# Optimization experiments

Hardware: AMD Instinct MI355X
Metric: run time of the kernel (lower is better)

## Reference

```python
import jax, jax.numpy as jnp
import numpy as np

N_SRC = 100_000
N_NODES = 1_000_000
N_NEIGH = 20
RAW_DIM = 256
NEIGH_DIM = 128
MSG_DIM = 128


def setup_inputs() -> dict:
    key = jax.random.key(0)
    ks = jax.random.split(key, 8)
    s = 0.05
    return {
        "raw_messages": jax.random.normal(ks[0], (N_SRC, RAW_DIM), dtype=jnp.float32),
        "neighbors": jax.random.randint(ks[1], (N_SRC, N_NEIGH), 0, N_NODES, dtype=jnp.int64),
        "memory": jax.random.normal(ks[2], (N_NODES, NEIGH_DIM), dtype=jnp.float32),
        "W1": jax.random.normal(ks[3], (RAW_DIM, RAW_DIM // 2), dtype=jnp.float32) * s,
        "b1": jnp.zeros((RAW_DIM // 2,), dtype=jnp.float32),
        "W2": jax.random.normal(ks[4], (RAW_DIM // 2, MSG_DIM), dtype=jnp.float32) * s,
        "b2": jnp.zeros((MSG_DIM,), dtype=jnp.float32),
        "Wn": jax.random.normal(ks[5], (NEIGH_DIM, MSG_DIM), dtype=jnp.float32) * s,
        "bn": jnp.zeros((MSG_DIM,), dtype=jnp.float32),
    }


def reference(raw_messages, neighbors, memory, W1, b1, W2, b2, Wn, bn):
    # Gather neighbor memories: [N, K, D_neigh]
    neighbor_memories = memory[neighbors]
    # Mean-pool over the K sampled neighbors: [N, D_neigh]
    neighbor_agg = neighbor_memories.mean(axis=1)
    # message_sum MLP: Linear -> ReLU -> Linear -> ReLU
    h = jax.nn.relu(raw_messages @ W1 + b1)
    a = jax.nn.relu(h @ W2 + b2)
    # neighbor_sum MLP: Linear -> ReLU
    b = jax.nn.relu(neighbor_agg @ Wn + bn)
    return a + b
```

## Files before the change

### kernel.cpp

```cpp
#include <hip/hip_runtime.h>

#define N_SRC   100000
#define N_NEIGH 20
#define DRAW    256
#define DH      128
#define DMSG    128
#define DNEI    128
#define LDS_PAD 8

typedef __bf16 bf16x8 __attribute__((ext_vector_type(8)));
typedef float  floatx4 __attribute__((ext_vector_type(4)));

__global__ void convert_weights(const float* __restrict__ W1,
                                const float* __restrict__ W2,
                                const float* __restrict__ Wn,
                                __bf16* __restrict__ W1t,
                                __bf16* __restrict__ W2t,
                                __bf16* __restrict__ Wnt) {
    int i = blockIdx.x * 256 + threadIdx.x;
    if (i < 32768) {
        int n = i >> 8, k = i & 255;
        W1t[i] = (__bf16)W1[k * 128 + n];
    } else if (i < 49152) {
        int j = i - 32768;
        int n = j >> 7, k = j & 127;
        W2t[j] = (__bf16)W2[k * 128 + n];
    } else {
        int j = i - 49152;
        int n = j >> 7, k = j & 127;
        Wnt[j] = (__bf16)Wn[k * 128 + n];
    }
}

__global__ __launch_bounds__(256)
void fused_kernel(const float* __restrict__ raw,
                  const int*   __restrict__ neigh,
                  const float* __restrict__ memv,
                  const float* __restrict__ b1,
                  const float* __restrict__ b2,
                  const float* __restrict__ bn,
                  const __bf16* __restrict__ W1t,
                  const __bf16* __restrict__ W2t,
                  const __bf16* __restrict__ Wnt,
                  float* __restrict__ out) {
    __shared__ __bf16 agg [64][DNEI + LDS_PAD];
    __shared__ __bf16 hbuf[64][DH   + LDS_PAD];

    const int tid = threadIdx.x;
    const int s0  = blockIdx.x * 64;

    {
        const int grp = tid >> 5;
        const int l32 = tid & 31;
        for (int sl = grp; sl < 64; sl += 8) {
            const int s = s0 + sl;
            float4 acc = make_float4(0.f, 0.f, 0.f, 0.f);
            if (s < N_SRC) {
                int myidx = 0;
                if (l32 < N_NEIGH) myidx = neigh[s * N_NEIGH + l32];
                #pragma unroll
                for (int n = 0; n < N_NEIGH; ++n) {
                    int idx = __shfl(myidx, n, 32);
                    const float4* row =
                        reinterpret_cast<const float4*>(memv + (size_t)idx * DNEI);
                    float4 v = row[l32];
                    acc.x += v.x; acc.y += v.y; acc.z += v.z; acc.w += v.w;
                }
                const float inv = 1.0f / N_NEIGH;
                acc.x *= inv; acc.y *= inv; acc.z *= inv; acc.w *= inv;
            }
            __bf16* dst = &agg[sl][l32 * 4];
            dst[0] = (__bf16)acc.x; dst[1] = (__bf16)acc.y;
            dst[2] = (__bf16)acc.z; dst[3] = (__bf16)acc.w;
        }
    }

    const int lane = tid & 63;
    const int wave = tid >> 6;
    const int mr   = lane & 15;
    const int quad = lane >> 4;

    {
        int rowg = s0 + wave * 16 + mr;
        int rowc = rowg < N_SRC ? rowg : N_SRC - 1;
        const float* ar = raw + (size_t)rowc * DRAW;

        floatx4 acc[8];
        #pragma unroll
        for (int nt = 0; nt < 8; ++nt) { floatx4 z = {0.f,0.f,0.f,0.f}; acc[nt] = z; }

        #pragma unroll
        for (int kk = 0; kk < DRAW; kk += 32) {
            const int kb = kk + quad * 8;
            float4 a0 = *reinterpret_cast<const float4*>(ar + kb);
            float4 a1 = *reinterpret_cast<const float4*>(ar + kb + 4);
            bf16x8 af;
            af[0]=(__bf16)a0.x; af[1]=(__bf16)a0.y; af[2]=(__bf16)a0.z; af[3]=(__bf16)a0.w;
            af[4]=(__bf16)a1.x; af[5]=(__bf16)a1.y; af[6]=(__bf16)a1.z; af[7]=(__bf16)a1.w;
            #pragma unroll
            for (int nt = 0; nt < 8; ++nt) {
                bf16x8 bf = *reinterpret_cast<const bf16x8*>(
                    W1t + (nt * 16 + mr) * DRAW + kb);
                acc[nt] = __builtin_amdgcn_mfma_f32_16x16x32_bf16(af, bf, acc[nt], 0, 0, 0);
            }
        }
        #pragma unroll
        for (int nt = 0; nt < 8; ++nt) {
            const int col  = nt * 16 + mr;
            const float bias = b1[col];
            #pragma unroll
            for (int r = 0; r < 4; ++r) {
                int mrow = wave * 16 + quad * 4 + r;
                float v = acc[nt][r] + bias;
                hbuf[mrow][col] = (__bf16)(v > 0.f ? v : 0.f);
            }
        }
    }

    __syncthreads();

    {
        floatx4 acc2[8], acc3[8];
        #pragma unroll
        for (int nt = 0; nt < 8; ++nt) {
            floatx4 z = {0.f,0.f,0.f,0.f}; acc2[nt] = z; acc3[nt] = z;
        }

        #pragma unroll
        for (int kk = 0; kk < DH; kk += 32) {
            const int kb = kk + quad * 8;
            bf16x8 af2 = *reinterpret_cast<const bf16x8*>(&hbuf[wave * 16 + mr][kb]);
            bf16x8 af3 = *reinterpret_cast<const bf16x8*>(&agg [wave * 16 + mr][kb]);
            #pragma unroll
            for (int nt = 0; nt < 8; ++nt) {
                bf16x8 bw2 = *reinterpret_cast<const bf16x8*>(
                    W2t + (nt * 16 + mr) * DH + kb);
                acc2[nt] = __builtin_amdgcn_mfma_f32_16x16x32_bf16(af2, bw2, acc2[nt], 0, 0, 0);
                bf16x8 bw3 = *reinterpret_cast<const bf16x8*>(
                    Wnt + (nt * 16 + mr) * DNEI + kb);
                acc3[nt] = __builtin_amdgcn_mfma_f32_16x16x32_bf16(af3, bw3, acc3[nt], 0, 0, 0);
            }
        }

        #pragma unroll
        for (int nt = 0; nt < 8; ++nt) {
            const int col = nt * 16 + mr;
            const float bb2 = b2[col];
            const float bbn = bn[col];
            #pragma unroll
            for (int r = 0; r < 4; ++r) {
                int rowl = wave * 16 + quad * 4 + r;
                int rowg = s0 + rowl;
                if (rowg < N_SRC) {
                    float va = acc2[nt][r] + bb2; va = va > 0.f ? va : 0.f;
                    float vb = acc3[nt][r] + bbn; vb = vb > 0.f ? vb : 0.f;
                    out[(size_t)rowg * DMSG + col] = va + vb;
                }
            }
        }
    }
}

extern "C" void kernel_launch(void* const* d_in, const int* in_sizes, int n_in,
                              void* d_out, int out_size, void* d_ws, size_t ws_size,
                              hipStream_t stream) {
    const float* raw   = (const float*)d_in[0];
    const int*   neigh = (const int*)  d_in[1];
    const float* memv  = (const float*)d_in[2];
    const float* W1    = (const float*)d_in[3];
    const float* b1    = (const float*)d_in[4];
    const float* W2    = (const float*)d_in[5];
    const float* b2    = (const float*)d_in[6];
    const float* Wn    = (const float*)d_in[7];
    const float* bn    = (const float*)d_in[8];
    float* out = (float*)d_out;

    __bf16* W1t = (__bf16*)d_ws;
    __bf16* W2t = W1t + 32768;
    __bf16* Wnt = W2t + 16384;

    convert_weights<<<dim3(256), dim3(256), 0, stream>>>(W1, W2, Wn, W1t, W2t, Wnt);

    const int nblocks = (N_SRC + 63) / 64;
    fused_kernel<<<dim3(nblocks), dim3(256), 0, stream>>>(
        raw, neigh, memv, b1, b2, bn, W1t, W2t, Wnt, out);
}
```

Measured before the change: 888.7 us.

## Split neighbor gather into separate kernel with batched loads, stage aggregate in workspace

Moves the neighbor gather and mean into a standalone kernel that issues ten independent row loads at a time per 32-lane group, then writes a bf16 aggregate buffer to the workspace. A second kernel runs the MLPs and reads that aggregate into shared memory. The goal is more memory-level parallelism on the random gather, which dominates the traffic, and decoupling it from the MFMA work. In exchange it adds an extra launch plus a write and read of a 25 MB bf16 intermediate, and it falls back to the fused kernel when the workspace is too small.

```diff
diff --git a/kernel.cpp b/kernel.cpp
--- a/kernel.cpp
+++ b/kernel.cpp
@@ -9,6 +9,7 @@
 #define LDS_PAD 8
 
 typedef __bf16 bf16x8 __attribute__((ext_vector_type(8)));
+typedef __bf16 bf16x4 __attribute__((ext_vector_type(4)));
 typedef float  floatx4 __attribute__((ext_vector_type(4)));
 
 __global__ void convert_weights(const float* __restrict__ W1,
@@ -33,6 +34,151 @@
 }
 
 __global__ __launch_bounds__(256)
+void gather_kernel(const int* __restrict__ neigh,
+                   const float* __restrict__ memv,
+                   __bf16* __restrict__ agg) {
+    const int gid = (blockIdx.x * 256 + threadIdx.x) >> 5;
+    const int l32 = threadIdx.x & 31;
+    if (gid >= N_SRC) return;
+
+    int myidx = 0;
+    if (l32 < N_NEIGH) myidx = neigh[gid * N_NEIGH + l32];
+
+    float4 acc = make_float4(0.f, 0.f, 0.f, 0.f);
+    float4 v[10];
+    #pragma unroll
+    for (int b = 0; b < 2; ++b) {
+        #pragma unroll
+        for (int j = 0; j < 10; ++j) {
+            int idx = __shfl(myidx, b * 10 + j, 32);
+            v[j] = reinterpret_cast<const float4*>(memv + (size_t)idx * DNEI)[l32];
+        }
+        #pragma unroll
+        for (int j = 0; j < 10; ++j) {
+            acc.x += v[j].x; acc.y += v[j].y; acc.z += v[j].z; acc.w += v[j].w;
+        }
+    }
+    const float inv = 1.0f / N_NEIGH;
+    bf16x4 o;
+    o[0] = (__bf16)(acc.x * inv); o[1] = (__bf16)(acc.y * inv);
+    o[2] = (__bf16)(acc.z * inv); o[3] = (__bf16)(acc.w * inv);
+    *reinterpret_cast<bf16x4*>(agg + (size_t)gid * DNEI + l32 * 4) = o;
+}
+
+__global__ __launch_bounds__(256)
+void mlp_kernel(const float* __restrict__ raw,
+                const __bf16* __restrict__ aggG,
+                const float* __restrict__ b1,
+                const float* __restrict__ b2,
+                const float* __restrict__ bn,
+                const __bf16* __restrict__ W1t,
+                const __bf16* __restrict__ W2t,
+                const __bf16* __restrict__ Wnt,
+                float* __restrict__ out) {
+    __shared__ __bf16 agg [64][DNEI + LDS_PAD];
+    __shared__ __bf16 hbuf[64][DH   + LDS_PAD];
+
+    const int tid = threadIdx.x;
+    const int s0  = blockIdx.x * 64;
+
+    {
+        #pragma unroll
+        for (int c = tid; c < 64 * 16; c += 256) {
+            int r = c >> 4, off = (c & 15) * 8;
+            if (s0 + r < N_SRC) {
+                *reinterpret_cast<bf16x8*>(&agg[r][off]) =
+                    *reinterpret_cast<const bf16x8*>(aggG + (size_t)(s0 + r) * DNEI + off);
+            }
+        }
+    }
+
+    const int lane = tid & 63;
+    const int wave = tid >> 6;
+    const int mr   = lane & 15;
+    const int quad = lane >> 4;
+
+    {
+        int rowg = s0 + wave * 16 + mr;
+        int rowc = rowg < N_SRC ? rowg : N_SRC - 1;
+        const float* ar = raw + (size_t)rowc * DRAW;
+
+        floatx4 acc[8];
+        #pragma unroll
+        for (int nt = 0; nt < 8; ++nt) { floatx4 z = {0.f,0.f,0.f,0.f}; acc[nt] = z; }
+
+        #pragma unroll
+        for (int kk = 0; kk < DRAW; kk += 32) {
+            const int kb = kk + quad * 8;
+            float4 a0 = *reinterpret_cast<const float4*>(ar + kb);
+            float4 a1 = *reinterpret_cast<const float4*>(ar + kb + 4);
+            bf16x8 af;
+            af[0]=(__bf16)a0.x; af[1]=(__bf16)a0.y; af[2]=(__bf16)a0.z; af[3]=(__bf16)a0.w;
+            af[4]=(__bf16)a1.x; af[5]=(__bf16)a1.y; af[6]=(__bf16)a1.z; af[7]=(__bf16)a1.w;
+            #pragma unroll
+            for (int nt = 0; nt < 8; ++nt) {
+                bf16x8 bf = *reinterpret_cast<const bf16x8*>(
+                    W1t + (nt * 16 + mr) * DRAW + kb);
+                acc[nt] = __builtin_amdgcn_mfma_f32_16x16x32_bf16(af, bf, acc[nt], 0, 0, 0);
+            }
+        }
+        #pragma unroll
+        for (int nt = 0; nt < 8; ++nt) {
+            const int col  = nt * 16 + mr;
+            const float bias = b1[col];
+            #pragma unroll
+            for (int r = 0; r < 4; ++r) {
+                int mrow = wave * 16 + quad * 4 + r;
+                float v = acc[nt][r] + bias;
+                hbuf[mrow][col] = (__bf16)(v > 0.f ? v : 0.f);
+            }
+        }
+    }
+
+    __syncthreads();
+
+    {
+        floatx4 acc2[8], acc3[8];
+        #pragma unroll
+        for (int nt = 0; nt < 8; ++nt) {
+            floatx4 z = {0.f,0.f,0.f,0.f}; acc2[nt] = z; acc3[nt] = z;
+        }
+
+        #pragma unroll
+        for (int kk = 0; kk < DH; kk += 32) {
+            const int kb = kk + quad * 8;
+            bf16x8 af2 = *reinterpret_cast<const bf16x8*>(&hbuf[wave * 16 + mr][kb]);
+            bf16x8 af3 = *reinterpret_cast<const bf16x8*>(&agg [wave * 16 + mr][kb]);
+            #pragma unroll
+            for (int nt = 0; nt < 8; ++nt) {
+                bf16x8 bw2 = *reinterpret_cast<const bf16x8*>(
+                    W2t + (nt * 16 + mr) * DH + kb);
+                acc2[nt] = __builtin_amdgcn_mfma_f32_16x16x32_bf16(af2, bw2, acc2[nt], 0, 0, 0);
+                bf16x8 bw3 = *reinterpret_cast<const bf16x8*>(
+                    Wnt + (nt * 16 + mr) * DNEI + kb);
+                acc3[nt] = __builtin_amdgcn_mfma_f32_16x16x32_bf16(af3, bw3, acc3[nt], 0, 0, 0);
+            }
+        }
+
+        #pragma unroll
+        for (int nt = 0; nt < 8; ++nt) {
+            const int col = nt * 16 + mr;
+            const float bb2 = b2[col];
+            const float bbn = bn[col];
+            #pragma unroll
+            for (int r = 0; r < 4; ++r) {
+                int rowl = wave * 16 + quad * 4 + r;
+                int rowg = s0 + rowl;
+                if (rowg < N_SRC) {
+                    float va = acc2[nt][r] + bb2; va = va > 0.f ? va : 0.f;
+                    float vb = acc3[nt][r] + bbn; vb = vb > 0.f ? vb : 0.f;
+                    out[(size_t)rowg * DMSG + col] = va + vb;
+                }
+            }
+        }
+    }
+}
+
+__global__ __launch_bounds__(256)
 void fused_kernel(const float* __restrict__ raw,
                   const int*   __restrict__ neigh,
                   const float* __restrict__ memv,
@@ -178,10 +324,19 @@
     __bf16* W1t = (__bf16*)d_ws;
     __bf16* W2t = W1t + 32768;
     __bf16* Wnt = W2t + 16384;
+    __bf16* agg = Wnt + 16384;
+    const size_t ws_needed = (size_t)(32768 + 16384 + 16384 + (size_t)N_SRC * DNEI) * 2;
 
     convert_weights<<<dim3(256), dim3(256), 0, stream>>>(W1, W2, Wn, W1t, W2t, Wnt);
 
-    const int nblocks = (N_SRC + 63) / 64;
-    fused_kernel<<<dim3(nblocks), dim3(256), 0, stream>>>(
-        raw, neigh, memv, b1, b2, bn, W1t, W2t, Wnt, out);
-}
+    const int nblocks_mlp = (N_SRC + 63) / 64;
+    if (ws_size >= ws_needed) {
+        const int nblocks_g = (N_SRC * 32 + 255) / 256;
+        gather_kernel<<<dim3(nblocks_g), dim3(256), 0, stream>>>(neigh, memv, agg);
+        mlp_kernel<<<dim3(nblocks_mlp), dim3(256), 0, stream>>>(
+            raw, agg, b1, b2, bn, W1t, W2t, Wnt, out);
+    } else {
+        fused_kernel<<<dim3(nblocks_mlp), dim3(256), 0, stream>>>(
+            raw, neigh, memv, b1, b2, bn, W1t, W2t, Wnt, out);
+    }
+}
```

Result: no change. 904.7 us (+1.8%).
